# Performance work log

Hardware: AMD Instinct MI355X
Metric: run time of the kernel (lower is better)

Reference implementation:

```python
import jax, jax.numpy as jnp
import numpy as np

_SAMPLING_EPS = 1e-5


def setup_inputs() -> dict:
    key = jax.random.key(0)
    ks = jax.random.split(key, 7)
    N, V, H = 256, 128000, 200  # num_seqs, vocab_size, output-history length
    logits = jax.random.normal(ks[0], (N, V), dtype=jnp.float32)
    output_tokens = jax.random.randint(ks[1], (N, H), 0, V, dtype=jnp.int32)
    presence_penalties = jax.random.uniform(ks[2], (N,), jnp.float32, 0.0, 2.0)
    frequency_penalties = jax.random.uniform(ks[3], (N,), jnp.float32, 0.0, 2.0)
    temperatures = jax.random.uniform(ks[4], (N,), jnp.float32, 0.5, 1.5)
    top_ps = jax.random.uniform(ks[5], (N,), jnp.float32, 0.5, 1.0)
    top_ks = jax.random.randint(ks[6], (N,), 1, 1000, dtype=jnp.int32)
    return {
        "logits": logits,
        "presence_penalties": presence_penalties,
        "frequency_penalties": frequency_penalties,
        "temperatures": temperatures,
        "top_ps": top_ps,
        "output_tokens": output_tokens,
        "top_ks": top_ks,
    }


def reference(logits, presence_penalties, frequency_penalties, temperatures,
              top_ps, output_tokens, top_ks):
    N, V = logits.shape

    # ---- _apply_penalties: bincount of previously generated tokens per row ----
    rows = jnp.arange(N)[:, None]  # [N,1] broadcast against [N,H] token ids
    bin_counts = jnp.zeros((N, V), logits.dtype).at[rows, output_tokens].add(1.0)
    # rows are skipped when both penalties are < eps (original builds an index list)
    active = ((presence_penalties >= _SAMPLING_EPS) |
              (frequency_penalties >= _SAMPLING_EPS))[:, None]
    presence_mask = (bin_counts > 0.0).astype(logits.dtype)
    penalty = (frequency_penalties[:, None] * bin_counts
               + presence_penalties[:, None] * presence_mask)
    logits = logits - jnp.where(active, penalty, jnp.zeros((), logits.dtype))

    # ---- temperature scaling + softmax ----
    logits = logits / temperatures[:, None]
    probs = jax.nn.softmax(logits, axis=-1)

    # ---- _apply_top_p_top_k: sort desc, cumsum, mask, unsort ----
    probs_idx = jnp.argsort(-probs, axis=-1)                    # descending order
    probs_sort = jnp.take_along_axis(probs, probs_idx, axis=-1)
    probs_sum = jnp.cumsum(probs_sort, axis=-1)
    top_p_mask = (probs_sum - probs_sort) > top_ps[:, None]     # exclusive cumsum > p
    probs_sort = jnp.where(top_p_mask, 0.0, probs_sort)
    top_k_mask = jnp.arange(V, dtype=top_ks.dtype)[None, :] >= top_ks[:, None]
    probs_sort = jnp.where(top_k_mask, 0.0, probs_sort)
    inv_idx = jnp.argsort(probs_idx, axis=-1)                   # unsort permutation
    filtered_probs = jnp.take_along_axis(probs_sort, inv_idx, axis=-1)
    return filtered_probs
```

## Files before the change

kernel.cpp:

```cpp
#include <hip/hip_runtime.h>
#include <stdint.h>

#define NBR 1024
#define BASEB 0x1700
#define BSHIFT 19
#define HS 512
#define HM 511
#define CAP 4096
#define CAP2 6144
#define NT 1024
#define CAPTHR 1.75f

typedef unsigned long long ull;

__device__ __forceinline__ void bar_lds() {
    asm volatile("s_waitcnt lgkmcnt(0)" ::: "memory");
    __builtin_amdgcn_s_barrier();
    __builtin_amdgcn_sched_barrier(0);
}
__device__ __forceinline__ void bar_full() {
    asm volatile("s_waitcnt vmcnt(0) lgkmcnt(0)" ::: "memory");
    __builtin_amdgcn_s_barrier();
    __builtin_amdgcn_sched_barrier(0);
}

__device__ __forceinline__ unsigned mono_u32(float x) {
    unsigned b = __float_as_uint(x);
    return (b & 0x80000000u) ? ~b : (b | 0x80000000u);
}
__device__ __forceinline__ float inv_mono(unsigned u) {
    unsigned b = (u & 0x80000000u) ? (u & 0x7fffffffu) : ~u;
    return __uint_as_float(b);
}
__device__ __forceinline__ int relb(unsigned m) {
    int rel = (int)(m >> BSHIFT) - BASEB;
    return rel < 0 ? 0 : (rel > NBR - 1 ? NBR - 1 : rel);
}

__device__ __forceinline__ float compute_x(float l, int cnt,
                                           float pres, float freq, float t) {
    float pen = __fadd_rn(__fmul_rn(freq, (float)cnt), (cnt > 0) ? pres : 0.0f);
    return __fdiv_rn(__fsub_rn(l, pen), t);
}

#define SHFL_STAGE(kk, jj) do {                                              \
    int _s = (jj) >> 1;                                                      \
    ull _pA = __shfl_xor(A, _s), _pB = __shfl_xor(B, _s);                    \
    bool _keepmn = (((e0 & (jj)) == 0) == ((e0 & (kk)) != 0));               \
    ull _mnA = (A < _pA) ? A : _pA, _mxA = (A < _pA) ? _pA : A;              \
    ull _mnB = (B < _pB) ? B : _pB, _mxB = (B < _pB) ? _pB : B;              \
    A = _keepmn ? _mnA : _mxA;  B = _keepmn ? _mnB : _mxB;                   \
} while (0)
#define PAIR_STAGE(kk) do {                                                  \
    bool _up = ((e0 & (kk)) != 0);                                           \
    ull _mn = (A < B) ? A : B, _mx = (A < B) ? B : A;                        \
    A = _up ? _mn : _mx;  B = _up ? _mx : _mn;                               \
} while (0)
#define ZDRIB(nn) do {                                                       \
    for (int _z = 0; _z < (nn) && zc < ZITER; ++_z) {                        \
        int _p = tid + zc * NT; if (_p < V4) o4p[_p] = z4; ++zc;             \
    }                                                                        \
} while (0)

__global__ __launch_bounds__(NT) void k_fused(
    const float* __restrict__ logits, const int* __restrict__ tokens,
    const float* __restrict__ pres_v, const float* __restrict__ freq_v,
    const float* __restrict__ temps, const float* __restrict__ topp_v,
    const int* __restrict__ topk_v, int V, int H, float* __restrict__ out)
{
    __shared__ __align__(16) char smem[56 * 1024];
    ull* cbuf = (ull*)smem;
    float* se = (float*)(smem + 32 * 1024);
    unsigned* hc = (unsigned*)(smem + 48 * 1024);
    int* hkey = (int*)(smem + 52 * 1024);
    int* hval = (int*)(smem + 54 * 1024);
    __shared__ int wt_i[16];
    __shared__ float wt_f[16];
    __shared__ float esum_s, corr_s;
    __shared__ int bstar_s, lcnt_s, cap_s;

    int row = blockIdx.x, tid = threadIdx.x;
    int lane = tid & 63, wid = tid >> 6;
    hc[tid] = 0u;
    if (tid == 0) { esum_s = 0.f; corr_s = 0.f; bstar_s = -1; lcnt_s = 0; cap_s = 0; }

    for (int i = tid; i < HS; i += NT) { hkey[i] = -1; hval[i] = 0; }
    __syncthreads();
    const int* trow = tokens + (size_t)row * H;
    for (int i = tid; i < H; i += NT) {
        int v = trow[i];
        unsigned h = ((unsigned)v * 2654435761u) >> 23;
        while (true) {
            int prev = atomicCAS(&hkey[h], -1, v);
            if (prev == -1 || prev == v) { atomicAdd(&hval[h], 1); break; }
            h = (h + 1) & HM;
        }
    }
    __syncthreads();

    float t = temps[row], topp = topp_v[row];
    float pres = pres_v[row], freq = freq_v[row];
    int k = topk_v[row];
    int active = (pres >= 1e-5f) || (freq >= 1e-5f);
    float r = __fdiv_rn(1.0f, t);
    const float* lrow = logits + (size_t)row * V;
    const float4* l4p = (const float4*)lrow;
    float4* o4p = (float4*)(out + (size_t)row * V);
    const float4 z4 = make_float4(0.f, 0.f, 0.f, 0.f);
    int V4 = V >> 2;
    int ZITER = (V4 + NT - 1) / NT;
    int zc = 0;

    float corr = 0.0f;
    if (active) {
        for (int s = tid; s < HS; s += NT) {
            int v = hkey[s];
            if (v >= 0) {
                int c = hval[s];
                float l = lrow[v];
                corr += __expf(compute_x(l, c, pres, freq, t))
                      - __expf(__fmul_rn(l, r));
            }
        }
    }
    for (int off = 32; off; off >>= 1) corr += __shfl_down(corr, off);
    if ((tid & 63) == 0) atomicAdd(&corr_s, corr);
    __syncthreads();

    float es = 0.0f;
    int i = tid;
    for (; i + 7 * NT < V4; i += 8 * NT) {
        float4 arr[8];
#pragma unroll
        for (int q = 0; q < 8; ++q) arr[q] = l4p[i + q * NT];
        __builtin_amdgcn_sched_barrier(0);
        ZDRIB(8);
#pragma unroll
        for (int q = 0; q < 8; ++q) {
            int vb = (i + q * NT) << 2;
#pragma unroll
            for (int j = 0; j < 4; ++j) {
                float l = (&arr[q].x)[j];
                es += __expf(__fmul_rn(l, r));
                if (l >= CAPTHR) {
                    unsigned idx = (unsigned)(vb + j);
                    int c = 0;
                    if (active) {
                        unsigned h = (idx * 2654435761u) >> 23;
                        while (true) {
                            int kk2 = hkey[h];
                            if (kk2 == (int)idx) { c = hval[h]; break; }
                            if (kk2 == -1) break;
                            h = (h + 1) & HM;
                        }
                    }
                    float xe = (c > 0) ? compute_x(l, c, pres, freq, t)
                                       : __fdiv_rn(l, t);
                    unsigned ue = mono_u32(xe);
                    atomicAdd(&hc[relb(ue)], 1u);
                    int pos = atomicAdd(&cap_s, 1);
                    if (pos < CAP2) cbuf[pos] = ((ull)ue << 32) | (unsigned)~idx;
                }
            }
        }
    }
    for (; i < V4; i += NT) {
        float4 A4 = l4p[i];
        __builtin_amdgcn_sched_barrier(0);
        ZDRIB(2);
#pragma unroll
        for (int j = 0; j < 4; ++j) {
            float l = (&A4.x)[j];
            es += __expf(__fmul_rn(l, r));
            if (l >= CAPTHR) {
                unsigned idx = (unsigned)((i << 2) + j);
                int c = 0;
                if (active) {
                    unsigned h = (idx * 2654435761u) >> 23;
                    while (true) {
                        int kk2 = hkey[h];
                        if (kk2 == (int)idx) { c = hval[h]; break; }
                        if (kk2 == -1) break;
                        h = (h + 1) & HM;
                    }
                }
                float xe = (c > 0) ? compute_x(l, c, pres, freq, t)
                                   : __fdiv_rn(l, t);
                unsigned ue = mono_u32(xe);
                atomicAdd(&hc[relb(ue)], 1u);
                int pos = atomicAdd(&cap_s, 1);
                if (pos < CAP2) cbuf[pos] = ((ull)ue << 32) | (unsigned)~idx;
            }
        }
    }
    for (int v = (V4 << 2) + tid; v < V; v += NT) {
        float l = lrow[v];
        es += __expf(__fmul_rn(l, r));
        if (l >= CAPTHR) {
            unsigned idx = (unsigned)v;
            int c = 0;
            if (active) {
                unsigned h = (idx * 2654435761u) >> 23;
                while (true) {
                    int kk2 = hkey[h];
                    if (kk2 == (int)idx) { c = hval[h]; break; }
                    if (kk2 == -1) break;
                    h = (h + 1) & HM;
                }
            }
            float xe = (c > 0) ? compute_x(l, c, pres, freq, t) : __fdiv_rn(l, t);
            unsigned ue = mono_u32(xe);
            atomicAdd(&hc[relb(ue)], 1u);
            int pos = atomicAdd(&cap_s, 1);
            if (pos < CAP2) cbuf[pos] = ((ull)ue << 32) | (unsigned)~idx;
        }
    }
    for (; zc < ZITER; ++zc) { int p = tid + zc * NT; if (p < V4) o4p[p] = z4; }
    for (int v2 = (V4 << 2) + tid; v2 < V; v2 += NT) out[(size_t)row * V + v2] = 0.0f;

    for (int off = 32; off; off >>= 1) es += __shfl_down(es, off);
    if ((tid & 63) == 0) atomicAdd(&esum_s, es);
    bar_lds();

    int myc = (int)hc[tid];
    int vscan = myc;
#pragma unroll
    for (int off = 1; off < 64; off <<= 1) {
        int o = __shfl_down(vscan, off);
        if (lane + off < 64) vscan += o;
    }
    if (lane == 0) wt_i[wid] = vscan;
    bar_lds();
    int tot = 0;
#pragma unroll
    for (int w = 0; w < 16; ++w) tot += wt_i[w];
    int above = vscan - myc;
#pragma unroll
    for (int w = 0; w < 16; ++w) if (w > wid) above += wt_i[w];
    int fb = (tot < k);
    if (!fb && (myc + above >= k)) atomicMax(&bstar_s, tid);
    bar_lds();
    int bst_rel = bstar_s; if (bst_rel < 0) bst_rel = 0;
    float Sp = esum_s + corr_s;
    int ccount = cap_s;
    int lb_rel = relb(mono_u32(__fdiv_rn(CAPTHR, t)));
    bool skip_c = (!fb) && (ccount <= CAP2) && (lb_rel < bst_rel);
    unsigned bst_abs = (unsigned)(bst_rel + BASEB);
    int count;

    if (skip_c) {
        int base6 = tid * 6;
        ull pr[6]; int sb[6]; int svc = 0;
#pragma unroll
        for (int q = 0; q < 6; ++q) {
            int j2 = base6 + q;
            bool in = (j2 < ccount);
            pr[q] = in ? cbuf[j2] : 0ull;
            int s = (in && (((unsigned)(pr[q] >> 32)) >> BSHIFT) >= bst_abs) ? 1 : 0;
            sb[q] = s; svc += s;
        }
        bar_lds();
        int vs = svc;
#pragma unroll
        for (int off = 1; off < 64; off <<= 1) {
            int o = __shfl_up(vs, off);
            if (lane >= off) vs += o;
        }
        if (lane == 63) wt_i[wid] = vs;
        bar_lds();
        int pre = vs - svc;
#pragma unroll
        for (int w = 0; w < 16; ++w) if (w < wid) pre += wt_i[w];
        int total = 0;
#pragma unroll
        for (int w = 0; w < 16; ++w) total += wt_i[w];
        int pos = pre;
#pragma unroll
        for (int q = 0; q < 6; ++q) if (sb[q]) cbuf[pos++] = pr[q];
        count = total > CAP ? CAP : total;
        bar_lds();
    } else {
        if (fb) {
            for (int v = tid; v < V; v += NT) {
                float l = lrow[v];
                if (!(l >= CAPTHR)) {
                    int c = 0;
                    if (active) {
                        unsigned h = ((unsigned)v * 2654435761u) >> 23;
                        while (true) {
                            int kk2 = hkey[h];
                            if (kk2 == v) { c = hval[h]; break; }
                            if (kk2 == -1) break;
                            h = (h + 1) & HM;
                        }
                    }
                    float xe = (c > 0) ? compute_x(l, c, pres, freq, t) : __fdiv_rn(l, t);
                    atomicAdd(&hc[relb(mono_u32(xe))], 1u);
                }
            }
            bar_lds();
            myc = (int)hc[tid];
            vscan = myc;
#pragma unroll
            for (int off = 1; off < 64; off <<= 1) {
                int o = __shfl_down(vscan, off);
                if (lane + off < 64) vscan += o;
            }
            if (lane == 0) wt_i[wid] = vscan;
            bar_lds();
            above = vscan - myc;
#pragma unroll
            for (int w = 0; w < 16; ++w) if (w > wid) above += wt_i[w];
            if (myc + above >= k) atomicMax(&bstar_s, tid);
            bar_lds();
            bst_rel = bstar_s < 0 ? 0 : bstar_s;
        }
        for (int v = tid; v < V; v += NT) {
            float l = lrow[v];
            int c = 0;
            if (active) {
                unsigned h = ((unsigned)v * 2654435761u) >> 23;
                while (true) {
                    int kk2 = hkey[h];
                    if (kk2 == v) { c = hval[h]; break; }
                    if (kk2 == -1) break;
                    h = (h + 1) & HM;
                }
            }
            float xe = (c > 0) ? compute_x(l, c, pres, freq, t) : __fdiv_rn(l, t);
            unsigned ue = mono_u32(xe);
            if (relb(ue) >= bst_rel) {
                int pos = atomicAdd(&lcnt_s, 1);
                if (pos < CAP) cbuf[pos] = ((ull)ue << 32) | (unsigned)~(unsigned)v;
            }
        }
        bar_lds();
        count = lcnt_s > CAP ? CAP : lcnt_s;
    }

    if (count <= 2048) {
        const int M = 2048;
        for (int j = count + tid; j < M; j += NT) cbuf[j] = 0ull;
        bar_lds();
        int e0 = (wid << 7) + (lane << 1);
        ull A = cbuf[e0], B = cbuf[e0 + 1];
        for (int kk = 2; kk <= 128; kk <<= 1) {
            for (int jj = kk >> 1; jj >= 2; jj >>= 1) SHFL_STAGE(kk, jj);
            PAIR_STAGE(kk);
        }
        for (int kk = 256; kk <= 2048; kk <<= 1) {
            cbuf[e0] = A; cbuf[e0 + 1] = B;
            bar_lds();
            for (int jj = kk >> 1; jj >= 128; jj >>= 1) {
                for (int i2 = tid; i2 < M; i2 += NT) {
                    int ixj = i2 ^ jj;
                    if (ixj > i2) {
                        ull X = cbuf[i2], Y = cbuf[ixj];
                        bool up = ((i2 & kk) != 0);
                        if ((X > Y) == up) { cbuf[i2] = Y; cbuf[ixj] = X; }
                    }
                }
                bar_lds();
            }
            A = cbuf[e0]; B = cbuf[e0 + 1];
            for (int jj = 64; jj >= 2; jj >>= 1) SHFL_STAGE(kk, jj);
            PAIR_STAGE(kk);
        }
        cbuf[e0] = A; cbuf[e0 + 1] = B;
        bar_lds();
    } else {
        int m = 1; while (m < count) m <<= 1;
        for (int j = count + tid; j < m; j += NT) cbuf[j] = 0ull;
        bar_lds();
        for (int kk = 2; kk <= m; kk <<= 1) {
            for (int jj = kk >> 1; jj > 0; jj >>= 1) {
                for (int i2 = tid; i2 < m; i2 += NT) {
                    int ixj = i2 ^ jj;
                    if (ixj > i2) {
                        ull X = cbuf[i2], Y = cbuf[ixj];
                        bool up = ((i2 & kk) != 0);
                        if ((X > Y) == up) { cbuf[i2] = Y; cbuf[ixj] = X; }
                    }
                }
                bar_lds();
            }
        }
    }

    for (int j = tid; j < CAP; j += NT)
        se[j] = (j < count) ? __expf(inv_mono((unsigned)(cbuf[j] >> 32))) : 0.0f;
    bar_lds();
    int j0 = tid << 2;
    float e0f = se[j0], e1 = se[j0 + 1], e2 = se[j0 + 2], e3 = se[j0 + 3];
    float c0 = e0f, c1 = c0 + e1, c2 = c1 + e2, c3 = c2 + e3;
    float vf = c3;
#pragma unroll
    for (int off = 1; off < 64; off <<= 1) {
        float o = __shfl_up(vf, off);
        if (lane >= off) vf += o;
    }
    if (lane == 63) wt_f[wid] = vf;
    bar_lds();
    float pre = vf - c3;
#pragma unroll
    for (int w = 0; w < 16; ++w) if (w < wid) pre += wt_f[w];

    bar_full();

    float pS = topp * Sp;
    float inc[4] = {pre + c0, pre + c1, pre + c2, pre + c3};
    float ee[4] = {e0f, e1, e2, e3};
#pragma unroll
    for (int q = 0; q < 4; ++q) {
        int j = j0 + q;
        if (j < count) {
            float e = ee[q];
            float excl = __fsub_rn(inc[q], e);
            if ((j < k) && (excl <= pS)) {
                unsigned idx = ~(unsigned)(cbuf[j] & 0xffffffffull);
                out[(size_t)row * V + idx] = __fdiv_rn(e, Sp);
            }
        }
    }
}

extern "C" void kernel_launch(void* const* d_in, const int* in_sizes, int n_in,
                              void* d_out, int out_size, void* d_ws, size_t ws_size,
                              hipStream_t stream) {
    const float* logits = (const float*)d_in[0];
    const float* pres   = (const float*)d_in[1];
    const float* freq   = (const float*)d_in[2];
    const float* temps  = (const float*)d_in[3];
    const float* topps  = (const float*)d_in[4];
    const int*   tokens = (const int*)d_in[5];
    const int*   topks  = (const int*)d_in[6];
    int N = in_sizes[1];
    int V = in_sizes[0] / N;
    int H = in_sizes[5] / N;
    float* out = (float*)d_out;

    k_fused<<<N, NT, 0, stream>>>(logits, tokens, pres, freq, temps, topps,
                                  topks, V, H, out);
}
```

Before: 305.0 us.

## Split fused kernel into parallel streaming pass and per-row select kernel

Replaces the single per-row fused kernel with three launches: an init kernel, a streaming kernel that reads each row across 8 blocks of 256 threads, accumulates the exp-sum and writes candidate (logit, index) pairs to global workspace, and a select kernel that loads the candidates, applies penalties, histograms, sorts and writes output. The goal is to raise parallelism for the bandwidth-bound logit scan beyond one block per row (256 blocks). The output zeroing moves to after the sort, and the candidate pairs now take a global round trip. This adds launch overhead and global atomics per row, and it falls back to a full rescan if workspace capacity is exceeded.

```diff
diff --git a/kernel.cpp b/kernel.cpp
--- a/kernel.cpp
+++ b/kernel.cpp
@@ -1,14 +1,16 @@
 #include <hip/hip_runtime.h>
 #include <stdint.h>
 
+#define BSHIFT 19
 #define NBR 1024
 #define BASEB 0x1700
-#define BSHIFT 19
 #define HS 512
 #define HM 511
 #define CAP 4096
-#define CAP2 6144
+#define CAPW 6144
 #define NT 1024
+#define NT1 256
+#define CH 8
 #define CAPTHR 1.75f
 
 typedef unsigned long long ull;
@@ -41,6 +43,17 @@
                                            float pres, float freq, float t) {
     float pen = __fadd_rn(__fmul_rn(freq, (float)cnt), (cnt > 0) ? pres : 0.0f);
     return __fdiv_rn(__fsub_rn(l, pen), t);
+}
+
+__device__ __forceinline__ int hash_cnt(unsigned idx, const int* hkey,
+                                        const int* hval) {
+    unsigned h = (idx * 2654435761u) >> 23;
+    while (true) {
+        int kk = hkey[h];
+        if (kk == (int)idx) return hval[h];
+        if (kk == -1) return 0;
+        h = (h + 1) & HM;
+    }
 }
 
 #define SHFL_STAGE(kk, jj) do {                                              \
@@ -62,30 +75,99 @@
     }                                                                        \
 } while (0)
 
-__global__ __launch_bounds__(NT) void k_fused(
+__global__ void k_init(float* esum, int* cur, int N) {
+    for (int i = threadIdx.x; i < N; i += blockDim.x) { esum[i] = 0.f; cur[i] = 0; }
+}
+
+__global__ __launch_bounds__(NT1) void k_stream(
+    const float* __restrict__ logits, const float* __restrict__ temps,
+    float* __restrict__ esum_ws, int* __restrict__ cur_ws,
+    ull* __restrict__ pairs, int capw, int V)
+{
+    int row = blockIdx.y, c = blockIdx.x, tid = threadIdx.x;
+    int V4 = V >> 2;
+    int csz = (V4 + CH - 1) / CH;
+    int beg = c * csz, end = beg + csz; if (end > V4) end = V4;
+    const float* lrow = logits + (size_t)row * V;
+    const float4* l4p = (const float4*)lrow;
+    ull* prow = pairs + (size_t)row * (size_t)capw;
+    float t = temps[row];
+    float r = __fdiv_rn(1.0f, t);
+    float es = 0.0f;
+    int i = beg + tid;
+    for (; i + 7 * NT1 < end; i += 8 * NT1) {
+        float4 arr[8];
+#pragma unroll
+        for (int q = 0; q < 8; ++q) arr[q] = l4p[i + q * NT1];
+#pragma unroll
+        for (int q = 0; q < 8; ++q) {
+            int vb = (i + q * NT1) << 2;
+#pragma unroll
+            for (int j = 0; j < 4; ++j) {
+                float l = (&arr[q].x)[j];
+                es += __expf(__fmul_rn(l, r));
+                if (l >= CAPTHR) {
+                    int pos = atomicAdd(&cur_ws[row], 1);
+                    if (pos < capw)
+                        prow[pos] = ((ull)__float_as_uint(l) << 32) | (unsigned)(vb + j);
+                }
+            }
+        }
+    }
+    for (; i < end; i += NT1) {
+        float4 A4 = l4p[i];
+        int vb = i << 2;
+#pragma unroll
+        for (int j = 0; j < 4; ++j) {
+            float l = (&A4.x)[j];
+            es += __expf(__fmul_rn(l, r));
+            if (l >= CAPTHR) {
+                int pos = atomicAdd(&cur_ws[row], 1);
+                if (pos < capw)
+                    prow[pos] = ((ull)__float_as_uint(l) << 32) | (unsigned)(vb + j);
+            }
+        }
+    }
+    if (c == CH - 1) {
+        for (int v = (V4 << 2) + tid; v < V; v += NT1) {
+            float l = lrow[v];
+            es += __expf(__fmul_rn(l, r));
+            if (l >= CAPTHR) {
+                int pos = atomicAdd(&cur_ws[row], 1);
+                if (pos < capw)
+                    prow[pos] = ((ull)__float_as_uint(l) << 32) | (unsigned)v;
+            }
+        }
+    }
+    for (int off = 32; off; off >>= 1) es += __shfl_down(es, off);
+    if ((tid & 63) == 0) atomicAdd(&esum_ws[row], es);
+}
+
+__global__ __launch_bounds__(NT) void k_select(
     const float* __restrict__ logits, const int* __restrict__ tokens,
     const float* __restrict__ pres_v, const float* __restrict__ freq_v,
     const float* __restrict__ temps, const float* __restrict__ topp_v,
-    const int* __restrict__ topk_v, int V, int H, float* __restrict__ out)
+    const int* __restrict__ topk_v, int V, int H, float* __restrict__ out,
+    const float* __restrict__ esum_ws, const int* __restrict__ cur_ws,
+    const ull* __restrict__ pairs, int capw)
 {
-    __shared__ __align__(16) char smem[56 * 1024];
-    ull* cbuf = (ull*)smem;
-    float* se = (float*)(smem + 32 * 1024);
-    unsigned* hc = (unsigned*)(smem + 48 * 1024);
-    int* hkey = (int*)(smem + 52 * 1024);
-    int* hval = (int*)(smem + 54 * 1024);
+    __shared__ __align__(16) ull sbuf[CAP];
+    __shared__ float se[CAP];
+    __shared__ unsigned hc[NBR];
+    __shared__ int hkey[HS];
+    __shared__ int hval[HS];
     __shared__ int wt_i[16];
     __shared__ float wt_f[16];
-    __shared__ float esum_s, corr_s;
-    __shared__ int bstar_s, lcnt_s, cap_s;
+    __shared__ float corr_s;
+    __shared__ int bstar_s, lcnt_s;
 
     int row = blockIdx.x, tid = threadIdx.x;
     int lane = tid & 63, wid = tid >> 6;
     hc[tid] = 0u;
-    if (tid == 0) { esum_s = 0.f; corr_s = 0.f; bstar_s = -1; lcnt_s = 0; cap_s = 0; }
-
+    if (tid == 0) { corr_s = 0.f; bstar_s = -1; lcnt_s = 0; }
     for (int i = tid; i < HS; i += NT) { hkey[i] = -1; hval[i] = 0; }
     __syncthreads();
+
     const int* trow = tokens + (size_t)row * H;
     for (int i = tid; i < H; i += NT) {
         int v = trow[i];
@@ -104,12 +186,22 @@
     int active = (pres >= 1e-5f) || (freq >= 1e-5f);
     float r = __fdiv_rn(1.0f, t);
     const float* lrow = logits + (size_t)row * V;
-    const float4* l4p = (const float4*)lrow;
     float4* o4p = (float4*)(out + (size_t)row * V);
     const float4 z4 = make_float4(0.f, 0.f, 0.f, 0.f);
     int V4 = V >> 2;
     int ZITER = (V4 + NT - 1) / NT;
     int zc = 0;
+    float esv = esum_ws[row];
+    int raw = cur_ws[row];
+    int ccount = raw < capw ? raw : capw;
+    const ull* prow = pairs + (size_t)row * (size_t)capw;
+
+    ull pr[6];
+#pragma unroll
+    for (int q = 0; q < 6; ++q) {
+        int j2 = tid + q * NT;
+        pr[q] = (j2 < ccount) ? prow[j2] : 0xffffffffffffffffull;
+    }
 
     float corr = 0.0f;
     if (active) {
@@ -127,148 +219,60 @@
     if ((tid & 63) == 0) atomicAdd(&corr_s, corr);
     __syncthreads();
 
-    float es = 0.0f;
-    int i = tid;
-    for (; i + 7 * NT < V4; i += 8 * NT) {
-        float4 arr[8];
-#pragma unroll
-        for (int q = 0; q < 8; ++q) arr[q] = l4p[i + q * NT];
-        __builtin_amdgcn_sched_barrier(0);
-        ZDRIB(8);
-#pragma unroll
-        for (int q = 0; q < 8; ++q) {
-            int vb = (i + q * NT) << 2;
-#pragma unroll
-            for (int j = 0; j < 4; ++j) {
-                float l = (&arr[q].x)[j];
-                es += __expf(__fmul_rn(l, r));
-                if (l >= CAPTHR) {
-                    unsigned idx = (unsigned)(vb + j);
-                    int c = 0;
-                    if (active) {
-                        unsigned h = (idx * 2654435761u) >> 23;
-                        while (true) {
-                            int kk2 = hkey[h];
-                            if (kk2 == (int)idx) { c = hval[h]; break; }
-                            if (kk2 == -1) break;
-                            h = (h + 1) & HM;
-                        }
-                    }
-                    float xe = (c > 0) ? compute_x(l, c, pres, freq, t)
-                                       : __fdiv_rn(l, t);
-                    unsigned ue = mono_u32(xe);
-                    atomicAdd(&hc[relb(ue)], 1u);
-                    int pos = atomicAdd(&cap_s, 1);
-                    if (pos < CAP2) cbuf[pos] = ((ull)ue << 32) | (unsigned)~idx;
-                }
-            }
-        }
-    }
-    for (; i < V4; i += NT) {
-        float4 A4 = l4p[i];
-        __builtin_amdgcn_sched_barrier(0);
-        ZDRIB(2);
-#pragma unroll
-        for (int j = 0; j < 4; ++j) {
-            float l = (&A4.x)[j];
-            es += __expf(__fmul_rn(l, r));
-            if (l >= CAPTHR) {
-                unsigned idx = (unsigned)((i << 2) + j);
-                int c = 0;
-                if (active) {
-                    unsigned h = (idx * 2654435761u) >> 23;
-                    while (true) {
-                        int kk2 = hkey[h];
-                        if (kk2 == (int)idx) { c = hval[h]; break; }
-                        if (kk2 == -1) break;
-                        h = (h + 1) & HM;
-                    }
-                }
-                float xe = (c > 0) ? compute_x(l, c, pres, freq, t)
-                                   : __fdiv_rn(l, t);
-                unsigned ue = mono_u32(xe);
-                atomicAdd(&hc[relb(ue)], 1u);
-                int pos = atomicAdd(&cap_s, 1);
-                if (pos < CAP2) cbuf[pos] = ((ull)ue << 32) | (unsigned)~idx;
-            }
-        }
-    }
-    for (int v = (V4 << 2) + tid; v < V; v += NT) {
-        float l = lrow[v];
-        es += __expf(__fmul_rn(l, r));
-        if (l >= CAPTHR) {
-            unsigned idx = (unsigned)v;
-            int c = 0;
-            if (active) {
-                unsigned h = (idx * 2654435761u) >> 23;
-                while (true) {
-                    int kk2 = hkey[h];
-                    if (kk2 == (int)idx) { c = hval[h]; break; }
-                    if (kk2 == -1) break;
-                    h = (h + 1) & HM;
-                }
-            }
+    ull sk[6]; int rel6[6];
+#pragma unroll
+    for (int q = 0; q < 6; ++q) {
+        if (pr[q] != 0xffffffffffffffffull) {
+            unsigned idx = (unsigned)(pr[q] & 0xffffffffull);
+            float l = __uint_as_float((unsigned)(pr[q] >> 32));
+            int c = active ? hash_cnt(idx, hkey, hval) : 0;
             float xe = (c > 0) ? compute_x(l, c, pres, freq, t) : __fdiv_rn(l, t);
             unsigned ue = mono_u32(xe);
-            atomicAdd(&hc[relb(ue)], 1u);
-            int pos = atomicAdd(&cap_s, 1);
-            if (pos < CAP2) cbuf[pos] = ((ull)ue << 32) | (unsigned)~idx;
-        }
-    }
-    for (; zc < ZITER; ++zc) { int p = tid + zc * NT; if (p < V4) o4p[p] = z4; }
-    for (int v2 = (V4 << 2) + tid; v2 < V; v2 += NT) out[(size_t)row * V + v2] = 0.0f;
-
-    for (int off = 32; off; off >>= 1) es += __shfl_down(es, off);
-    if ((tid & 63) == 0) atomicAdd(&esum_s, es);
-    bar_lds();
+            int rl = relb(ue);
+            atomicAdd(&hc[rl], 1u);
+            sk[q] = ((ull)ue << 32) | (unsigned)~idx;
+            rel6[q] = rl;
+        } else { sk[q] = 0ull; rel6[q] = -1; }
+    }
+    ZDRIB(2); bar_lds();
 
     int myc = (int)hc[tid];
-    int vscan = myc;
+    int vs = myc;
 #pragma unroll
     for (int off = 1; off < 64; off <<= 1) {
-        int o = __shfl_down(vscan, off);
-        if (lane + off < 64) vscan += o;
-    }
-    if (lane == 0) wt_i[wid] = vscan;
-    bar_lds();
+        int o = __shfl_down(vs, off);
+        if (lane + off < 64) vs += o;
+    }
+    if (lane == 0) wt_i[wid] = vs;
+    ZDRIB(2); bar_lds();
     int tot = 0;
 #pragma unroll
     for (int w = 0; w < 16; ++w) tot += wt_i[w];
-    int above = vscan - myc;
+    int above = vs - myc;
 #pragma unroll
     for (int w = 0; w < 16; ++w) if (w > wid) above += wt_i[w];
-    int fb = (tot < k);
+    int fb = (tot < k) || (raw > capw) || (capw <= 0);
     if (!fb && (myc + above >= k)) atomicMax(&bstar_s, tid);
-    bar_lds();
-    int bst_rel = bstar_s; if (bst_rel < 0) bst_rel = 0;
-    float Sp = esum_s + corr_s;
-    int ccount = cap_s;
+    ZDRIB(2); bar_lds();
+    int bst_rel = bstar_s < 0 ? 0 : bstar_s;
     int lb_rel = relb(mono_u32(__fdiv_rn(CAPTHR, t)));
-    bool skip_c = (!fb) && (ccount <= CAP2) && (lb_rel < bst_rel);
-    unsigned bst_abs = (unsigned)(bst_rel + BASEB);
+    bool skip = (!fb) && (lb_rel < bst_rel);
+    float Sp = esv + corr_s;
     int count;
 
-    if (skip_c) {
-        int base6 = tid * 6;
-        ull pr[6]; int sb[6]; int svc = 0;
-#pragma unroll
-        for (int q = 0; q < 6; ++q) {
-            int j2 = base6 + q;
-            bool in = (j2 < ccount);
-            pr[q] = in ? cbuf[j2] : 0ull;
-            int s = (in && (((unsigned)(pr[q] >> 32)) >> BSHIFT) >= bst_abs) ? 1 : 0;
-            sb[q] = s; svc += s;
-        }
-        bar_lds();
-        int vs = svc;
+    if (skip) {
+        int sb[6], svc = 0;
+#pragma unroll
+        for (int q = 0; q < 6; ++q) { sb[q] = (rel6[q] >= bst_rel) ? 1 : 0; svc += sb[q]; }
+        int vp = svc;
 #pragma unroll
         for (int off = 1; off < 64; off <<= 1) {
-            int o = __shfl_up(vs, off);
-            if (lane >= off) vs += o;
-        }
-        if (lane == 63) wt_i[wid] = vs;
-        bar_lds();
-        int pre = vs - svc;
+            int o = __shfl_up(vp, off);
+            if (lane >= off) vp += o;
+        }
+        if (lane == 63) wt_i[wid] = vp;
+        ZDRIB(2); bar_lds();
+        int pre = vp - svc;
 #pragma unroll
         for (int w = 0; w < 16; ++w) if (w < wid) pre += wt_i[w];
         int total = 0;
@@ -276,62 +280,44 @@
         for (int w = 0; w < 16; ++w) total += wt_i[w];
         int pos = pre;
 #pragma unroll
-        for (int q = 0; q < 6; ++q) if (sb[q]) cbuf[pos++] = pr[q];
+        for (int q = 0; q < 6; ++q)
+            if (sb[q]) { if (pos < CAP) sbuf[pos] = sk[q]; ++pos; }
         count = total > CAP ? CAP : total;
-        bar_lds();
+        ZDRIB(2); bar_lds();
     } else {
-        if (fb) {
-            for (int v = tid; v < V; v += NT) {
-                float l = lrow[v];
-                if (!(l >= CAPTHR)) {
-                    int c = 0;
-                    if (active) {
-                        unsigned h = ((unsigned)v * 2654435761u) >> 23;
-                        while (true) {
-                            int kk2 = hkey[h];
-                            if (kk2 == v) { c = hval[h]; break; }
-                            if (kk2 == -1) break;
-                            h = (h + 1) & HM;
-                        }
-                    }
-                    float xe = (c > 0) ? compute_x(l, c, pres, freq, t) : __fdiv_rn(l, t);
-                    atomicAdd(&hc[relb(mono_u32(xe))], 1u);
-                }
-            }
-            bar_lds();
-            myc = (int)hc[tid];
-            vscan = myc;
-#pragma unroll
-            for (int off = 1; off < 64; off <<= 1) {
-                int o = __shfl_down(vscan, off);
-                if (lane + off < 64) vscan += o;
-            }
-            if (lane == 0) wt_i[wid] = vscan;
-            bar_lds();
-            above = vscan - myc;
-#pragma unroll
-            for (int w = 0; w < 16; ++w) if (w > wid) above += wt_i[w];
-            if (myc + above >= k) atomicMax(&bstar_s, tid);
-            bar_lds();
-            bst_rel = bstar_s < 0 ? 0 : bstar_s;
-        }
+        if (tid == 0) bstar_s = -1;
+        hc[tid] = 0u;
+        bar_lds();
         for (int v = tid; v < V; v += NT) {
             float l = lrow[v];
-            int c = 0;
-            if (active) {
-                unsigned h = ((unsigned)v * 2654435761u) >> 23;
-                while (true) {
-                    int kk2 = hkey[h];
-                    if (kk2 == v) { c = hval[h]; break; }
-                    if (kk2 == -1) break;
-                    h = (h + 1) & HM;
-                }
-            }
+            int c = active ? hash_cnt((unsigned)v, hkey, hval) : 0;
+            float xe = (c > 0) ? compute_x(l, c, pres, freq, t) : __fdiv_rn(l, t);
+            atomicAdd(&hc[relb(mono_u32(xe))], 1u);
+        }
+        bar_lds();
+        myc = (int)hc[tid];
+        vs = myc;
+#pragma unroll
+        for (int off = 1; off < 64; off <<= 1) {
+            int o = __shfl_down(vs, off);
+            if (lane + off < 64) vs += o;
+        }
+        if (lane == 0) wt_i[wid] = vs;
+        bar_lds();
+        above = vs - myc;
+#pragma unroll
+        for (int w = 0; w < 16; ++w) if (w > wid) above += wt_i[w];
+        if (myc + above >= k) atomicMax(&bstar_s, tid);
+        bar_lds();
+        bst_rel = bstar_s < 0 ? 0 : bstar_s;
+        for (int v = tid; v < V; v += NT) {
+            float l = lrow[v];
+            int c = active ? hash_cnt((unsigned)v, hkey, hval) : 0;
             float xe = (c > 0) ? compute_x(l, c, pres, freq, t) : __fdiv_rn(l, t);
             unsigned ue = mono_u32(xe);
             if (relb(ue) >= bst_rel) {
                 int pos = atomicAdd(&lcnt_s, 1);
-                if (pos < CAP) cbuf[pos] = ((ull)ue << 32) | (unsigned)~(unsigned)v;
+                if (pos < CAP) sbuf[pos] = ((ull)ue << 32) | (unsigned)~(unsigned)v;
             }
         }
         bar_lds();
@@ -340,46 +326,46 @@
 
     if (count <= 2048) {
         const int M = 2048;
-        for (int j = count + tid; j < M; j += NT) cbuf[j] = 0ull;
-        bar_lds();
+        for (int j = count + tid; j < M; j += NT) sbuf[j] = 0ull;
+        ZDRIB(2); bar_lds();
         int e0 = (wid << 7) + (lane << 1);
-        ull A = cbuf[e0], B = cbuf[e0 + 1];
+        ull A = sbuf[e0], B = sbuf[e0 + 1];
+        ZDRIB(2);
         for (int kk = 2; kk <= 128; kk <<= 1) {
             for (int jj = kk >> 1; jj >= 2; jj >>= 1) SHFL_STAGE(kk, jj);
             PAIR_STAGE(kk);
         }
         for (int kk = 256; kk <= 2048; kk <<= 1) {
-            cbuf[e0] = A; cbuf[e0 + 1] = B;
-            bar_lds();
+            sbuf[e0] = A; sbuf[e0 + 1] = B;
+            ZDRIB(2); bar_lds();
             for (int jj = kk >> 1; jj >= 128; jj >>= 1) {
                 for (int i2 = tid; i2 < M; i2 += NT) {
                     int ixj = i2 ^ jj;
                     if (ixj > i2) {
-                        ull X = cbuf[i2], Y = cbuf[ixj];
+                        ull X = sbuf[i2], Y = sbuf[ixj];
                         bool up = ((i2 & kk) != 0);
-                        if ((X > Y) == up) { cbuf[i2] = Y; cbuf[ixj] = X; }
+                        if ((X > Y) == up) { sbuf[i2] = Y; sbuf[ixj] = X; }
                     }
                 }
-                bar_lds();
-            }
-            A = cbuf[e0]; B = cbuf[e0 + 1];
+                ZDRIB(2); bar_lds();
+            }
+            A = sbuf[e0]; B = sbuf[e0 + 1];
             for (int jj = 64; jj >= 2; jj >>= 1) SHFL_STAGE(kk, jj);
             PAIR_STAGE(kk);
         }
-        cbuf[e0] = A; cbuf[e0 + 1] = B;
-        bar_lds();
+        sbuf[e0] = A; sbuf[e0 + 1] = B;
     } else {
         int m = 1; while (m < count) m <<= 1;
-        for (int j = count + tid; j < m; j += NT) cbuf[j] = 0ull;
+        for (int j = count + tid; j < m; j += NT) sbuf[j] = 0ull;
         bar_lds();
         for (int kk = 2; kk <= m; kk <<= 1) {
             for (int jj = kk >> 1; jj > 0; jj >>= 1) {
                 for (int i2 = tid; i2 < m; i2 += NT) {
                     int ixj = i2 ^ jj;
                     if (ixj > i2) {
-                        ull X = cbuf[i2], Y = cbuf[ixj];
+                        ull X = sbuf[i2], Y = sbuf[ixj];
                         bool up = ((i2 & kk) != 0);
-                        if ((X > Y) == up) { cbuf[i2] = Y; cbuf[ixj] = X; }
+                        if ((X > Y) == up) { sbuf[i2] = Y; sbuf[ixj] = X; }
                     }
                 }
                 bar_lds();
@@ -387,8 +373,16 @@
         }
     }
 
+    for (; zc < ZITER; ++zc) {
+        int p = tid + zc * NT;
+        if (p < V4) o4p[p] = z4;
+    }
+    for (int v2 = (V4 << 2) + tid; v2 < V; v2 += NT)
+        out[(size_t)row * V + v2] = 0.0f;
+    bar_lds();
+
     for (int j = tid; j < CAP; j += NT)
-        se[j] = (j < count) ? __expf(inv_mono((unsigned)(cbuf[j] >> 32))) : 0.0f;
+        se[j] = (j < count) ? __expf(inv_mono((unsigned)(sbuf[j] >> 32))) : 0.0f;
     bar_lds();
     int j0 = tid << 2;
     float e0f = se[j0], e1 = se[j0 + 1], e2 = se[j0 + 2], e3 = se[j0 + 3];
@@ -417,7 +411,7 @@
             float e = ee[q];
             float excl = __fsub_rn(inc[q], e);
             if ((j < k) && (excl <= pS)) {
-                unsigned idx = ~(unsigned)(cbuf[j] & 0xffffffffull);
+                unsigned idx = ~(unsigned)(sbuf[j] & 0xffffffffull);
                 out[(size_t)row * V + idx] = __fdiv_rn(e, Sp);
             }
         }
@@ -439,6 +433,19 @@
     int H = in_sizes[5] / N;
     float* out = (float*)d_out;
 
-    k_fused<<<N, NT, 0, stream>>>(logits, tokens, pres, freq, temps, topps,
-                                  topks, V, H, out);
-}
+    size_t A = ((size_t)N * 4 + 255) & ~(size_t)255;
+    float* esum_ws = (float*)d_ws;
+    int*   cur_ws  = (int*)((char*)d_ws + A);
+    ull*   pairs   = (ull*)((char*)d_ws + 2 * A);
+    int capw = 0;
+    if (ws_size > 2 * A + 8)
+        capw = (int)(((ws_size - 2 * A) / 8) / (size_t)N);
+    if (capw > CAPW) capw = CAPW;
+    if (capw < 0) capw = 0;
+
+    k_init<<<1, 256, 0, stream>>>(esum_ws, cur_ws, N);
+    k_stream<<<dim3(CH, N), NT1, 0, stream>>>(logits, temps, esum_ws, cur_ws,
+                                              pairs, capw, V);
+    k_select<<<N, NT, 0, stream>>>(logits, tokens, pres, freq, temps, topps,
+                                   topks, V, H, out, esum_ws, cur_ws, pairs, capw);
+}
```

Result: slower. 875.9 us (+187.2%).
